# Performance work log

Hardware: AMD Instinct MI355X
Metric: run time of the kernel (lower is better)

The kernel has to match this reference:

```python
import jax, jax.numpy as jnp
import numpy as np
import math

HEADS = 16
HEAD_DIM = 64
DIM = 1024
B, S = 2, 2048
ROPE_THETA = 10000.0


def make_rope(seq_len):
    # Faithful to DitRotary.forward: theta over even indices, cos/sin duplicated per pair
    theta = 1.0 / ROPE_THETA ** (jnp.arange(0, HEAD_DIM, 2, dtype=jnp.float32) / HEAD_DIM)
    pos = jnp.arange(seq_len, dtype=jnp.float32)[:, None]          # [S,1]
    idx_theta = pos * theta                                         # [S,32]
    cs = jnp.stack([jnp.cos(idx_theta), jnp.sin(idx_theta)])        # [2,S,32]
    cs = jnp.stack((cs, cs), axis=-1).reshape(2, seq_len, HEAD_DIM) # duplicate pairs -> [2,S,64]
    return cs[:, None, :, None, :]                                   # [2,1,S,1,64]


def rotate_half(x):
    # interleaved pair rotation: (x0,x1)->(-x1,x0)
    xr = x.reshape(*x.shape[:-1], -1, 2)
    x1, x2 = xr[..., 0], xr[..., 1]
    return jnp.stack((-x2, x1), axis=-1).reshape(x.shape)


def setup_inputs() -> dict:
    key = jax.random.key(0)
    ks = jax.random.split(key, 10)
    sd = 1.0 / math.sqrt(DIM)
    x = jax.random.normal(ks[0], (B, S, DIM), dtype=jnp.float32)
    rope = make_rope(S)
    mask = jnp.zeros((1, 1, S, S), dtype=jnp.float32)
    Wq = jax.random.normal(ks[1], (DIM, DIM), dtype=jnp.float32) * sd
    bq = jax.random.normal(ks[2], (DIM,), dtype=jnp.float32) * 0.02
    Wk = jax.random.normal(ks[3], (DIM, DIM), dtype=jnp.float32) * sd
    bk = jax.random.normal(ks[4], (DIM,), dtype=jnp.float32) * 0.02
    Wv = jax.random.normal(ks[5], (DIM, DIM), dtype=jnp.float32) * sd
    bv = jax.random.normal(ks[6], (DIM,), dtype=jnp.float32) * 0.02
    Wo = jax.random.normal(ks[7], (DIM, DIM), dtype=jnp.float32) * sd
    bo = jax.random.normal(ks[8], (DIM,), dtype=jnp.float32) * 0.02
    return dict(x=x, rope=rope, mask=mask, Wq=Wq, bq=bq, Wk=Wk, bk=bk, Wv=Wv, bv=bv, Wo=Wo, bo=bo)


def reference(x, rope, mask, Wq, bq, Wk, bk, Wv, bv, Wo, bo):
    b, s, d = x.shape
    q = (x @ Wq + bq).reshape(b, s, HEADS, HEAD_DIM)
    k = (x @ Wk + bk).reshape(b, s, HEADS, HEAD_DIM)
    v = (x @ Wv + bv).reshape(b, s, HEADS, HEAD_DIM)
    cos, sin = rope[0], rope[1]          # [1,S,1,64], broadcasts over [B,S,H,D]
    q = q * cos + rotate_half(q) * sin
    k = k * cos + rotate_half(k) * sin
    scale = 1.0 / math.sqrt(HEAD_DIM)
    scores = jnp.einsum('bqhd,bkhd->bhqk', q, k) * scale + mask   # [B,H,S,S]
    attn = jax.nn.softmax(scores.astype(jnp.float32), axis=-1).astype(q.dtype)
    out = jnp.einsum('bhqk,bkhd->bqhd', attn, v).reshape(b, s, HEADS * HEAD_DIM)
    return out @ Wo + bo   # to_out[1] is Dropout -> identity at eval
```

## Files before the change

kernel.cpp:

```cpp
#include <hip/hip_runtime.h>
#include <hip/hip_bf16.h>

typedef unsigned short u16;
typedef unsigned int u32;
typedef __attribute__((ext_vector_type(8))) short short8;
typedef __attribute__((ext_vector_type(4))) short short4v;
typedef __attribute__((ext_vector_type(4))) float floatx4;
typedef __attribute__((ext_vector_type(16))) float floatx16;

#define DEVI __device__ __forceinline__

static constexpr int Bb  = 2;
static constexpr int Ss  = 2048;
static constexpr int Hh  = 16;
static constexpr int Dd  = 64;
static constexpr int DIM = 1024;
static constexpr int BH  = Bb * Hh;
static constexpr int MT  = Bb * Ss;

DEVI u16 f2bf(float f) {
  unsigned u = __float_as_uint(f);
  u = (u + 0x7fffu + ((u >> 16) & 1u)) >> 16;
  return (u16)u;
}
DEVI float bf2f(u16 h) { return __uint_as_float(((unsigned)h) << 16); }

DEVI void gload16(const void* g, void* l) {
  __builtin_amdgcn_global_load_lds(
      (const __attribute__((address_space(1))) unsigned*)g,
      (__attribute__((address_space(3))) unsigned*)l, 16, 0, 0);
}

DEVI floatx4 mfma16(short8 a, short8 b, floatx4 c) {
  return __builtin_amdgcn_mfma_f32_16x16x32_bf16(a, b, c, 0, 0, 0);
}
DEVI floatx16 mfma32(short8 a, short8 b, floatx16 c) {
  return __builtin_amdgcn_mfma_f32_32x32x16_bf16(a, b, c, 0, 0, 0);
}

__global__ void k_cvt(const float* __restrict__ x, u16* __restrict__ o, int n8) {
  int i = blockIdx.x * 256 + threadIdx.x;
  if (i >= n8) return;
  floatx4 a = *(const floatx4*)(x + (size_t)i * 8);
  floatx4 b = *(const floatx4*)(x + (size_t)i * 8 + 4);
  u16 r[8];
#pragma unroll
  for (int j = 0; j < 4; ++j) { r[j] = f2bf(a[j]); r[4 + j] = f2bf(b[j]); }
  *(short8*)(o + (size_t)i * 8) = *(short8*)r;
}

__global__ void k_wt(const float* __restrict__ Wq, const float* __restrict__ Wk,
                     const float* __restrict__ Wv, const float* __restrict__ Wo,
                     u16* __restrict__ wt) {
  __shared__ __align__(16) u16 L[64 * 65];
  int mat = blockIdx.z;
  const float* W = (mat == 0) ? Wq : (mat == 1) ? Wk : (mat == 2) ? Wv : Wo;
  int k0 = blockIdx.x * 64, n0 = blockIdx.y * 64;
  int t = threadIdx.x;
  int kr = t >> 4, nc = (t & 15) * 4;
#pragma unroll
  for (int i = 0; i < 4; ++i) {
    int kl = kr + i * 16;
    floatx4 v = *(const floatx4*)(W + (size_t)(k0 + kl) * DIM + n0 + nc);
    u16* d = L + kl * 65 + nc;
#pragma unroll
    for (int j = 0; j < 4; ++j) d[j] = f2bf(v[j]);
  }
  __syncthreads();
  int nr = t >> 4, kc = (t & 15) * 4;
#pragma unroll
  for (int i = 0; i < 4; ++i) {
    int nl = nr + i * 16;
    u16 r[4];
#pragma unroll
    for (int j = 0; j < 4; ++j) r[j] = L[(kc + j) * 65 + nl];
    *(short4v*)(wt + ((size_t)mat * DIM + n0 + nl) * DIM + k0 + kc) = *(short4v*)r;
  }
}

__global__ void k_rope(u16* __restrict__ x, const float* __restrict__ rope, float scale) {
  int g = blockIdx.x * 256 + threadIdx.x;
  int d0 = (g & 7) * 8;
  int s  = (g >> 3) & (Ss - 1);
  u16* p = x + (size_t)g * 8;
  short8 v = *(short8*)p;
  const float* cp = rope + (size_t)s * 64 + d0;
  const float* sp = cp + Ss * 64;
  u16 o[8];
#pragma unroll
  for (int i = 0; i < 4; ++i) {
    float c  = cp[2 * i];
    float sn = sp[2 * i];
    float x0 = bf2f((u16)v[2 * i]);
    float x1 = bf2f((u16)v[2 * i + 1]);
    o[2 * i]     = f2bf((x0 * c - x1 * sn) * scale);
    o[2 * i + 1] = f2bf((x1 * c + x0 * sn) * scale);
  }
  *(short8*)p = *(short8*)o;
}

template <int EPI>
__global__ __launch_bounds__(256, 2) void k_gemm(
    const u16* __restrict__ A, const u16* __restrict__ Bt,
    int M, int N, int K,
    const float* __restrict__ b0, const float* __restrict__ b1, const float* __restrict__ b2,
    float* __restrict__ Cf, u16* __restrict__ q_out, u16* __restrict__ k_out,
    u16* __restrict__ vt_out) {
  __shared__ __align__(16) u16 As[128 * 64];
  __shared__ __align__(16) u16 Bs[128 * 64];
  int t = threadIdx.x, lane = t & 63, w = t >> 6;
  int wr = w >> 1, wc = w & 1;
  int m0 = blockIdx.x * 128, n0 = blockIdx.y * 128;
  int rl = lane & 15, hl = lane >> 4;
  int sr = t >> 3, sc = t & 7;
  floatx4 acc[4][4] = {};
  int nk = K >> 6;
  for (int kt = 0; kt < nk; ++kt) {
#pragma unroll
    for (int i = 0; i < 4; ++i) {
      int row = i * 32 + sr;
      int cs = sc ^ (row & 7);
      gload16(A  + (size_t)(m0 + row) * K + kt * 64 + cs * 8, (char*)As + row * 128 + sc * 16);
      gload16(Bt + (size_t)(n0 + row) * K + kt * 64 + cs * 8, (char*)Bs + row * 128 + sc * 16);
    }
    asm volatile("s_waitcnt vmcnt(0)" ::: "memory");
    __syncthreads();
    short8 af[2][4], bfr[2][4];
#pragma unroll
    for (int kk = 0; kk < 2; ++kk) {
#pragma unroll
      for (int i = 0; i < 4; ++i) {
        int ra = wr * 64 + i * 16 + rl;
        af[kk][i] = *(const short8*)((const char*)As + ra * 128 + (((kk * 4 + hl) ^ (ra & 7)) * 16));
        int rb = wc * 64 + i * 16 + rl;
        bfr[kk][i] = *(const short8*)((const char*)Bs + rb * 128 + (((kk * 4 + hl) ^ (rb & 7)) * 16));
      }
    }
#pragma unroll
    for (int kk = 0; kk < 2; ++kk)
#pragma unroll
      for (int mi = 0; mi < 4; ++mi)
#pragma unroll
        for (int ni = 0; ni < 4; ++ni)
          acc[mi][ni] = mfma16(af[kk][mi], bfr[kk][ni], acc[mi][ni]);
    __syncthreads();
  }
  if (EPI == 0) {
#pragma unroll
    for (int mi = 0; mi < 4; ++mi)
#pragma unroll
      for (int ni = 0; ni < 4; ++ni) {
        int n = n0 + wc * 64 + ni * 16 + rl;
        float bias = b0[n];
#pragma unroll
        for (int r = 0; r < 4; ++r) {
          int m = m0 + wr * 64 + mi * 16 + hl * 4 + r;
          Cf[(size_t)m * N + n] = acc[mi][ni][r] + bias;
        }
      }
  } else {
    int mat = n0 >> 10;
    const float* bp = (mat == 0) ? b0 : (mat == 1) ? b1 : b2;
#pragma unroll
    for (int mi = 0; mi < 4; ++mi)
#pragma unroll
      for (int ni = 0; ni < 4; ++ni) {
        int nn = (n0 & 1023) + wc * 64 + ni * 16 + rl;
        float bias = bp[nn];
        int h = nn >> 6, d = nn & 63;
#pragma unroll
        for (int r = 0; r < 4; ++r) {
          int m = m0 + wr * 64 + mi * 16 + hl * 4 + r;
          int b = m >> 11, s = m & 2047;
          float v = acc[mi][ni][r] + bias;
          if (mat == 2)
            vt_out[(((size_t)b * Hh + h) * Dd + d) * Ss + s] = f2bf(v);
          else {
            u16* dst = (mat == 0) ? q_out : k_out;
            dst[(((size_t)b * Hh + h) * Ss + s) * Dd + d] = f2bf(v);
          }
        }
      }
  }
}

__global__ __launch_bounds__(256, 2) void k_attn(
    const u16* __restrict__ q, const u16* __restrict__ kk_,
    const u16* __restrict__ vt, u16* __restrict__ ao) {
  __shared__ __align__(16) u16 Ks[64 * 64];
  __shared__ __align__(16) u16 Vs[64 * 64];
  __shared__ float Ls[4 * 32];
  constexpr float NB2 = -17.3123405f;
  int t = threadIdx.x, lane = t & 63, w = t >> 6;
  int id = blockIdx.x;
  int swz = (id & 7) * 64 + (id >> 3);
  int bh = swz >> 4, q0 = (swz & 15) * 128;
  int ql = lane & 31, hi = lane >> 5;
  int sr = t >> 3, sc = t & 7;
  const u16* qrow = q + ((size_t)bh * Ss + q0 + w * 32 + ql) * Dd + hi * 8;
  short8 qf[4];
#pragma unroll
  for (int c = 0; c < 4; ++c) qf[c] = *(const short8*)(qrow + 16 * c);
  floatx16 oacc0 = {}, oacc1 = {};
  float lsum = 0.f;
  const u16* kbase = kk_ + (size_t)bh * Ss * Dd;
  const u16* vbase = vt + (size_t)bh * Dd * Ss;
  for (int kv0 = 0; kv0 < Ss; kv0 += 64) {
#pragma unroll
    for (int i = 0; i < 2; ++i) {
      int row = i * 32 + sr;
      int cs = sc ^ (row & 7);
      gload16(kbase + (size_t)(kv0 + row) * 64 + cs * 8, (char*)Ks + row * 128 + sc * 16);
      gload16(vbase + (size_t)row * Ss + kv0 + cs * 8, (char*)Vs + row * 128 + sc * 16);
    }
    asm volatile("s_waitcnt vmcnt(0)" ::: "memory");
    __syncthreads();
#pragma unroll
    for (int sub = 0; sub < 2; ++sub) {
      floatx16 sacc;
#pragma unroll
      for (int i = 0; i < 16; ++i) sacc[i] = NB2;
      int krow = sub * 32 + ql;
      const char* kr = (const char*)Ks + krow * 128;
#pragma unroll
      for (int c = 0; c < 4; ++c) {
        short8 kf = *(const short8*)(kr + (((2 * c + hi) ^ (krow & 7)) * 16));
        sacc = mfma32(kf, qf[c], sacc);
      }
      u32 c0[4], c1[4];
#pragma unroll
      for (int g = 0; g < 4; ++g) {
        float p0 = __builtin_amdgcn_exp2f(sacc[4 * g + 0]);
        float p1 = __builtin_amdgcn_exp2f(sacc[4 * g + 1]);
        float p2 = __builtin_amdgcn_exp2f(sacc[4 * g + 2]);
        float p3 = __builtin_amdgcn_exp2f(sacc[4 * g + 3]);
        lsum += (p0 + p1) + (p2 + p3);
        asm("v_cvt_pk_bf16_f32 %0, %1, %2" : "=v"(c0[g]) : "v"(p0), "v"(p1));
        asm("v_cvt_pk_bf16_f32 %0, %1, %2" : "=v"(c1[g]) : "v"(p2), "v"(p3));
      }
#pragma unroll
      for (int k2 = 0; k2 < 2; ++k2) {
        u32 a0 = c0[2 * k2], b0 = c0[2 * k2 + 1];
        u32 a1 = c1[2 * k2], b1 = c1[2 * k2 + 1];
        asm volatile("v_permlane32_swap_b32 %0, %1" : "+v"(a0), "+v"(b0));
        asm volatile("v_permlane32_swap_b32 %0, %1" : "+v"(a1), "+v"(b1));
        u32 fr[4] = {a0, a1, b0, b1};
        short8 pa = *(short8*)fr;
        int ks = sub * 2 + k2;
        int vr0 = ql;
        short8 vf0 = *(const short8*)((const char*)Vs + vr0 * 128 + (((2 * ks + hi) ^ (vr0 & 7)) * 16));
        oacc0 = mfma32(pa, vf0, oacc0);
        int vr1 = 32 + ql;
        short8 vf1 = *(const short8*)((const char*)Vs + vr1 * 128 + (((2 * ks + hi) ^ (vr1 & 7)) * 16));
        oacc1 = mfma32(pa, vf1, oacc1);
      }
    }
    __syncthreads();
  }
  float ltot = lsum + __shfl_xor(lsum, 32);
  if (hi == 0) Ls[w * 32 + ql] = 1.f / ltot;
  asm volatile("s_waitcnt lgkmcnt(0)" ::: "memory");
  int b = bh >> 4, h = bh & 15;
  u16* aobase = ao + ((size_t)b * Ss + q0 + w * 32) * DIM + h * 64 + ql;
#pragma unroll
  for (int g = 0; g < 4; ++g)
#pragma unroll
    for (int r4 = 0; r4 < 4; ++r4) {
      int reg = g * 4 + r4;
      int row = r4 + 8 * g + 4 * hi;
      float linv = Ls[w * 32 + row];
      aobase[(size_t)row * DIM]      = f2bf(oacc0[reg] * linv);
      aobase[(size_t)row * DIM + 32] = f2bf(oacc1[reg] * linv);
    }
}

extern "C" void kernel_launch(void* const* d_in, const int* in_sizes, int n_in,
                              void* d_out, int out_size, void* d_ws, size_t ws_size,
                              hipStream_t stream) {
  const float* x    = (const float*)d_in[0];
  const float* rope = (const float*)d_in[1];
  const float* Wq = (const float*)d_in[3];
  const float* bq = (const float*)d_in[4];
  const float* Wk = (const float*)d_in[5];
  const float* bk = (const float*)d_in[6];
  const float* Wv = (const float*)d_in[7];
  const float* bv = (const float*)d_in[8];
  const float* Wo = (const float*)d_in[9];
  const float* bo = (const float*)d_in[10];
  float* out = (float*)d_out;

  char* ws = (char*)d_ws;
  u16* xb = (u16*)ws;  ws += (size_t)MT * DIM * 2;
  u16* wt = (u16*)ws;  ws += (size_t)4 * DIM * DIM * 2;
  u16* qb = (u16*)ws;  ws += (size_t)BH * Ss * Dd * 2;
  u16* kb = (u16*)ws;  ws += (size_t)BH * Ss * Dd * 2;
  u16* vtb = (u16*)ws; ws += (size_t)BH * Dd * Ss * 2;
  u16* ao = xb;

  k_cvt<<<2048, 256, 0, stream>>>(x, xb, MT * DIM / 8);
  k_wt<<<dim3(16, 16, 4), 256, 0, stream>>>(Wq, Wk, Wv, Wo, wt);
  k_gemm<1><<<dim3(32, 24), 256, 0, stream>>>(xb, wt, MT, 3 * DIM, DIM,
                                              bq, bk, bv, nullptr, qb, kb, vtb);
  k_rope<<<2048, 256, 0, stream>>>(qb, rope, 0.18033688f);
  k_rope<<<2048, 256, 0, stream>>>(kb, rope, 1.0f);
  k_attn<<<512, 256, 0, stream>>>(qb, kb, vtb, ao);
  k_gemm<0><<<dim3(32, 8), 256, 0, stream>>>(ao, wt + (size_t)3 * DIM * DIM, MT, DIM, DIM,
                                             bo, nullptr, nullptr, out, nullptr, nullptr, nullptr);
  (void)in_sizes; (void)n_in; (void)out_size; (void)ws_size;
}
```

Before: 224.7 us.

## Fuse RoPE into QKV GEMM epilogue via LDS staging; double-buffer attention KV loads

Removes the two separate RoPE kernels by applying rotary embedding and the Q scale in the QKV GEMM epilogue. The accumulator tile is staged through shared memory, with a swapped MFMA operand order for the QKV path, so Q/K/V^T can be written with coalesced 16-byte stores instead of scattered 2-byte ones. The attention kernel double-buffers its K/V tiles in shared memory and overlaps the next tile's global loads with compute, using partial waitcnt and raw barriers. This doubles the attention kernel's LDS use, which could lower occupancy, and adds an extra barrier to the GEMM epilogue.

```diff
diff --git a/kernel.cpp b/kernel.cpp
--- a/kernel.cpp
+++ b/kernel.cpp
@@ -78,36 +78,17 @@
   }
 }
 
-__global__ void k_rope(u16* __restrict__ x, const float* __restrict__ rope, float scale) {
-  int g = blockIdx.x * 256 + threadIdx.x;
-  int d0 = (g & 7) * 8;
-  int s  = (g >> 3) & (Ss - 1);
-  u16* p = x + (size_t)g * 8;
-  short8 v = *(short8*)p;
-  const float* cp = rope + (size_t)s * 64 + d0;
-  const float* sp = cp + Ss * 64;
-  u16 o[8];
-#pragma unroll
-  for (int i = 0; i < 4; ++i) {
-    float c  = cp[2 * i];
-    float sn = sp[2 * i];
-    float x0 = bf2f((u16)v[2 * i]);
-    float x1 = bf2f((u16)v[2 * i + 1]);
-    o[2 * i]     = f2bf((x0 * c - x1 * sn) * scale);
-    o[2 * i + 1] = f2bf((x1 * c + x0 * sn) * scale);
-  }
-  *(short8*)p = *(short8*)o;
-}
-
 template <int EPI>
 __global__ __launch_bounds__(256, 2) void k_gemm(
     const u16* __restrict__ A, const u16* __restrict__ Bt,
     int M, int N, int K,
     const float* __restrict__ b0, const float* __restrict__ b1, const float* __restrict__ b2,
+    const float* __restrict__ rope,
     float* __restrict__ Cf, u16* __restrict__ q_out, u16* __restrict__ k_out,
     u16* __restrict__ vt_out) {
-  __shared__ __align__(16) u16 As[128 * 64];
-  __shared__ __align__(16) u16 Bs[128 * 64];
+  __shared__ __align__(16) u16 SH[2 * 128 * 64];
+  u16* As = SH;
+  u16* Bs = SH + 128 * 64;
   int t = threadIdx.x, lane = t & 63, w = t >> 6;
   int wr = w >> 1, wc = w & 1;
   int m0 = blockIdx.x * 128, n0 = blockIdx.y * 128;
@@ -141,8 +122,12 @@
 #pragma unroll
       for (int mi = 0; mi < 4; ++mi)
 #pragma unroll
-        for (int ni = 0; ni < 4; ++ni)
-          acc[mi][ni] = mfma16(af[kk][mi], bfr[kk][ni], acc[mi][ni]);
+        for (int ni = 0; ni < 4; ++ni) {
+          if (EPI == 1)
+            acc[mi][ni] = mfma16(bfr[kk][ni], af[kk][mi], acc[mi][ni]);
+          else
+            acc[mi][ni] = mfma16(af[kk][mi], bfr[kk][ni], acc[mi][ni]);
+        }
     __syncthreads();
   }
   if (EPI == 0) {
@@ -161,34 +146,82 @@
   } else {
     int mat = n0 >> 10;
     const float* bp = (mat == 0) ? b0 : (mat == 1) ? b1 : b2;
-#pragma unroll
-    for (int mi = 0; mi < 4; ++mi)
-#pragma unroll
-      for (int ni = 0; ni < 4; ++ni) {
-        int nn = (n0 & 1023) + wc * 64 + ni * 16 + rl;
-        float bias = bp[nn];
-        int h = nn >> 6, d = nn & 63;
-#pragma unroll
-        for (int r = 0; r < 4; ++r) {
-          int m = m0 + wr * 64 + mi * 16 + hl * 4 + r;
-          int b = m >> 11, s = m & 2047;
-          float v = acc[mi][ni][r] + bias;
-          if (mat == 2)
-            vt_out[(((size_t)b * Hh + h) * Dd + d) * Ss + s] = f2bf(v);
-          else {
-            u16* dst = (mat == 0) ? q_out : k_out;
-            dst[(((size_t)b * Hh + h) * Ss + s) * Dd + d] = f2bf(v);
+    float bv[4][4];
+#pragma unroll
+    for (int ni = 0; ni < 4; ++ni)
+#pragma unroll
+      for (int r = 0; r < 4; ++r)
+        bv[ni][r] = bp[(n0 & 1023) + wc * 64 + ni * 16 + hl * 4 + r];
+    char* T = (char*)SH;
+    if (mat < 2) {
+#pragma unroll
+      for (int mi = 0; mi < 4; ++mi)
+#pragma unroll
+        for (int ni = 0; ni < 4; ++ni) {
+          int m_loc = wr * 64 + mi * 16 + rl;
+          int cm = wc * 8 + ni * 2 + (hl >> 1);
+          u16 pk[4];
+#pragma unroll
+          for (int r = 0; r < 4; ++r) pk[r] = f2bf(acc[mi][ni][r] + bv[ni][r]);
+          *(short4v*)(T + m_loc * 256 + ((cm ^ (m_loc & 7)) << 4) + (hl & 1) * 8) = *(short4v*)pk;
+        }
+    } else {
+#pragma unroll
+      for (int mi = 0; mi < 4; ++mi)
+#pragma unroll
+        for (int ni = 0; ni < 4; ++ni) {
+          int m_loc = wr * 64 + mi * 16 + rl;
+          int mc = m_loc >> 3;
+#pragma unroll
+          for (int r = 0; r < 4; ++r) {
+            int n_loc = wc * 64 + ni * 16 + hl * 4 + r;
+            *(u16*)(T + n_loc * 256 + ((mc ^ (n_loc & 7)) << 4) + (m_loc & 7) * 2) =
+                f2bf(acc[mi][ni][r] + bv[ni][r]);
           }
         }
-      }
+    }
+    __syncthreads();
+    if (mat < 2) {
+      u16* dst = (mat == 0) ? q_out : k_out;
+      float sc2 = (mat == 0) ? 0.18033688f : 1.0f;
+#pragma unroll
+      for (int it = 0; it < 8; ++it) {
+        int g = it * 256 + t;
+        int row = g >> 4, c = g & 15;
+        short8 vv = *(const short8*)(T + row * 256 + ((c ^ (row & 7)) << 4));
+        int m = m0 + row, b = m >> 11, s = m & 2047;
+        int nn = (n0 & 1023) + c * 8, h = nn >> 6, d0 = nn & 63;
+        const float* cp = rope + (size_t)s * 64 + d0;
+        const float* sp = cp + (size_t)Ss * 64;
+        u16 o[8];
+#pragma unroll
+        for (int i2 = 0; i2 < 4; ++i2) {
+          float cc = cp[2 * i2], sn = sp[2 * i2];
+          float x0 = bf2f((u16)vv[2 * i2]), x1 = bf2f((u16)vv[2 * i2 + 1]);
+          o[2 * i2]     = f2bf((x0 * cc - x1 * sn) * sc2);
+          o[2 * i2 + 1] = f2bf((x1 * cc + x0 * sn) * sc2);
+        }
+        *(short8*)(dst + (((size_t)b * Hh + h) * Ss + s) * Dd + d0) = *(short8*)o;
+      }
+    } else {
+      int b = m0 >> 11, s0 = m0 & 2047;
+#pragma unroll
+      for (int it = 0; it < 8; ++it) {
+        int g = it * 256 + t;
+        int row = g >> 4, c = g & 15;
+        short8 vv = *(const short8*)(T + row * 256 + ((c ^ (row & 7)) << 4));
+        int nn = (n0 & 1023) + row, h = nn >> 6, d = nn & 63;
+        *(short8*)(vt_out + (((size_t)b * Hh + h) * Dd + d) * Ss + s0 + c * 8) = vv;
+      }
+    }
   }
 }
 
 __global__ __launch_bounds__(256, 2) void k_attn(
     const u16* __restrict__ q, const u16* __restrict__ kk_,
     const u16* __restrict__ vt, u16* __restrict__ ao) {
-  __shared__ __align__(16) u16 Ks[64 * 64];
-  __shared__ __align__(16) u16 Vs[64 * 64];
+  __shared__ __align__(16) u16 Ks[2][64 * 64];
+  __shared__ __align__(16) u16 Vs[2][64 * 64];
   __shared__ float Ls[4 * 32];
   constexpr float NB2 = -17.3123405f;
   int t = threadIdx.x, lane = t & 63, w = t >> 6;
@@ -205,23 +238,35 @@
   float lsum = 0.f;
   const u16* kbase = kk_ + (size_t)bh * Ss * Dd;
   const u16* vbase = vt + (size_t)bh * Dd * Ss;
-  for (int kv0 = 0; kv0 < Ss; kv0 += 64) {
+  auto stage = [&](int buf, int kv0) {
 #pragma unroll
     for (int i = 0; i < 2; ++i) {
       int row = i * 32 + sr;
       int cs = sc ^ (row & 7);
-      gload16(kbase + (size_t)(kv0 + row) * 64 + cs * 8, (char*)Ks + row * 128 + sc * 16);
-      gload16(vbase + (size_t)row * Ss + kv0 + cs * 8, (char*)Vs + row * 128 + sc * 16);
-    }
-    asm volatile("s_waitcnt vmcnt(0)" ::: "memory");
-    __syncthreads();
+      gload16(kbase + (size_t)(kv0 + row) * 64 + cs * 8, (char*)Ks[buf] + row * 128 + sc * 16);
+      gload16(vbase + (size_t)row * Ss + kv0 + cs * 8, (char*)Vs[buf] + row * 128 + sc * 16);
+    }
+  };
+  stage(0, 0);
+  for (int tt = 0; tt < 32; ++tt) {
+    int cur = tt & 1;
+    if (tt < 31) {
+      stage(cur ^ 1, (tt + 1) * 64);
+      asm volatile("s_waitcnt vmcnt(4)" ::: "memory");
+    } else {
+      asm volatile("s_waitcnt vmcnt(0)" ::: "memory");
+    }
+    __builtin_amdgcn_s_barrier();
+    asm volatile("" ::: "memory");
+    const char* kp = (const char*)Ks[cur];
+    const char* vp = (const char*)Vs[cur];
 #pragma unroll
     for (int sub = 0; sub < 2; ++sub) {
       floatx16 sacc;
 #pragma unroll
       for (int i = 0; i < 16; ++i) sacc[i] = NB2;
       int krow = sub * 32 + ql;
-      const char* kr = (const char*)Ks + krow * 128;
+      const char* kr = kp + krow * 128;
 #pragma unroll
       for (int c = 0; c < 4; ++c) {
         short8 kf = *(const short8*)(kr + (((2 * c + hi) ^ (krow & 7)) * 16));
@@ -248,14 +293,15 @@
         short8 pa = *(short8*)fr;
         int ks = sub * 2 + k2;
         int vr0 = ql;
-        short8 vf0 = *(const short8*)((const char*)Vs + vr0 * 128 + (((2 * ks + hi) ^ (vr0 & 7)) * 16));
+        short8 vf0 = *(const short8*)(vp + vr0 * 128 + (((2 * ks + hi) ^ (vr0 & 7)) * 16));
         oacc0 = mfma32(pa, vf0, oacc0);
         int vr1 = 32 + ql;
-        short8 vf1 = *(const short8*)((const char*)Vs + vr1 * 128 + (((2 * ks + hi) ^ (vr1 & 7)) * 16));
+        short8 vf1 = *(const short8*)(vp + vr1 * 128 + (((2 * ks + hi) ^ (vr1 & 7)) * 16));
         oacc1 = mfma32(pa, vf1, oacc1);
       }
     }
-    __syncthreads();
+    asm volatile("" ::: "memory");
+    __builtin_amdgcn_s_barrier();
   }
   float ltot = lsum + __shfl_xor(lsum, 32);
   if (hi == 0) Ls[w * 32 + ql] = 1.f / ltot;
@@ -300,11 +346,9 @@
   k_cvt<<<2048, 256, 0, stream>>>(x, xb, MT * DIM / 8);
   k_wt<<<dim3(16, 16, 4), 256, 0, stream>>>(Wq, Wk, Wv, Wo, wt);
   k_gemm<1><<<dim3(32, 24), 256, 0, stream>>>(xb, wt, MT, 3 * DIM, DIM,
-                                              bq, bk, bv, nullptr, qb, kb, vtb);
-  k_rope<<<2048, 256, 0, stream>>>(qb, rope, 0.18033688f);
-  k_rope<<<2048, 256, 0, stream>>>(kb, rope, 1.0f);
+                                              bq, bk, bv, rope, nullptr, qb, kb, vtb);
   k_attn<<<512, 256, 0, stream>>>(qb, kb, vtb, ao);
   k_gemm<0><<<dim3(32, 8), 256, 0, stream>>>(ao, wt + (size_t)3 * DIM * DIM, MT, DIM, DIM,
-                                             bo, nullptr, nullptr, out, nullptr, nullptr, nullptr);
+                                             bo, nullptr, nullptr, nullptr, out, nullptr, nullptr, nullptr);
   (void)in_sizes; (void)n_in; (void)out_size; (void)ws_size;
 }
```

Result: faster. 206.5 us (-8.1%).
